# Kernel tuning notes

Hardware: AMD Instinct MI355X
Metric: run time of the kernel (lower is better)

Reference implementation:

```python
import jax, jax.numpy as jnp
import numpy as np

HQ, HKV, HD = 16, 4, 64  # q heads, kv heads, head dim
ROPE_BASE = 10000.0


def _rope_tables(n, dim):
    inv_freq = 1.0 / (ROPE_BASE ** (jnp.arange(0, dim, 2, dtype=jnp.float32) / dim))
    t = jnp.arange(n, dtype=jnp.float32)
    freqs = jnp.outer(t, inv_freq)           # [N, dim/2]
    emb = jnp.concatenate([freqs, freqs], -1)  # [N, dim]
    return jnp.cos(emb), jnp.sin(emb)


def _rotate_half(x):
    h = x.shape[-1] // 2
    return jnp.concatenate([-x[..., h:], x[..., :h]], axis=-1)


def _apply_rope(x, cos, sin):
    # x: [B, N, H, D]; cos/sin: [N, D]
    c = cos[None, :, None, :]
    s = sin[None, :, None, :]
    return x * c + _rotate_half(x) * s


def setup_inputs() -> dict:
    key = jax.random.key(0)
    ks = jax.random.split(key, 5)
    B, N, D = 2, 4096, 1024
    kvD = HKV * HD
    sc = 0.02
    return {
        "x": jax.random.normal(ks[0], (B, N, D), jnp.float32),
        "Wq": jax.random.normal(ks[1], (D, D), jnp.float32) * sc,
        "Wk": jax.random.normal(ks[2], (D, kvD), jnp.float32) * sc,
        "Wv": jax.random.normal(ks[3], (D, kvD), jnp.float32) * sc,
        "Wo": jax.random.normal(ks[4], (D, D), jnp.float32) * sc,
    }


def reference(x, Wq, Wk, Wv, Wo):
    B, N, D = x.shape
    G = HQ // HKV
    Q = (x @ Wq).reshape(B, N, HQ, HD)
    K = (x @ Wk).reshape(B, N, HKV, HD)
    V = (x @ Wv).reshape(B, N, HKV, HD)

    cos, sin = _rope_tables(N, HD)
    Q = _apply_rope(Q, cos, sin)
    K = _apply_rope(K, cos, sin)

    # GQA: expand KV heads to match Q heads (repeat_interleave over head dim)
    K = jnp.repeat(K, G, axis=2)  # [B, N, HQ, HD]
    V = jnp.repeat(V, G, axis=2)

    Q = Q.transpose(0, 2, 1, 3)  # [B, HQ, N, HD]
    K = K.transpose(0, 2, 1, 3)
    V = V.transpose(0, 2, 1, 3)

    scores = jnp.einsum('bhqd,bhkd->bhqk', Q, K) / jnp.sqrt(jnp.float32(HD))
    attn = jax.nn.softmax(scores, axis=-1)
    out = jnp.einsum('bhqk,bhkd->bhqd', attn, V)  # [B, HQ, N, HD]
    out = out.transpose(0, 2, 1, 3).reshape(B, N, D)
    return out @ Wo
```

## Files before the change

### kernel.cpp

```cpp
#include <hip/hip_runtime.h>

#define HQn   16
#define HKVn  4
#define HDn   64
#define SEQN  4096
#define NB    2
#define DM    1024
#define KVD   256
#define NPACK 1536

#define QSCALE 0.18033688011112042f

typedef __attribute__((ext_vector_type(8))) short short8;
typedef __attribute__((ext_vector_type(4))) float f32x4;

#define MFMA16 __builtin_amdgcn_mfma_f32_16x16x32_bf16
#define EXP2F(x) __builtin_amdgcn_exp2f(x)

static __device__ __forceinline__ unsigned short f2bf(float f){
  union { float f; unsigned int u; } c; c.f = f;
  unsigned int r = c.u + 0x7fffu + ((c.u >> 16) & 1u);
  return (unsigned short)(r >> 16);
}

#if __has_builtin(__builtin_amdgcn_cvt_pk_bf16_f32)
typedef __attribute__((ext_vector_type(2))) __bf16 bf16x2v;
static __device__ __forceinline__ unsigned int pk_bf2(float a, float b){
  union { bf16x2v v; unsigned int u; } c;
  c.v = __builtin_amdgcn_cvt_pk_bf16_f32(a, b);
  return c.u;
}
#else
static __device__ __forceinline__ unsigned int pk_bf2(float a, float b){
  union { float f; unsigned int u; } ca, cb; ca.f = a; cb.f = b;
  return ((ca.u + 0x8000u) >> 16) | ((cb.u + 0x8000u) & 0xFFFF0000u);
}
#endif

static __device__ __forceinline__ void gl2lds16(const void* g, void* l){
  __builtin_amdgcn_global_load_lds(
      (const __attribute__((address_space(1))) void*)g,
      (__attribute__((address_space(3))) void*)l, 16, 0, 0);
}

__global__ void rope_tables_k(float* __restrict__ ct, float* __restrict__ st){
  int t = blockIdx.x, d = threadIdx.x;
  int i = d & 31;
  float inv = 1.0f / powf(10000.0f, (float)i * (1.0f/32.0f));
  float ang = (float)t * inv;
  ct[t*HDn + d] = cosf(ang);
  st[t*HDn + d] = sinf(ang);
}

__global__ __launch_bounds__(256) void castx_k(const float* __restrict__ x,
                                               unsigned short* __restrict__ xb){
  size_t i = ((size_t)blockIdx.x * 256 + threadIdx.x) * 8;
  float4 a = *(const float4*)(x + i);
  float4 b = *(const float4*)(x + i + 4);
  short8 o;
  o[0]=f2bf(a.x); o[1]=f2bf(a.y); o[2]=f2bf(a.z); o[3]=f2bf(a.w);
  o[4]=f2bf(b.x); o[5]=f2bf(b.y); o[6]=f2bf(b.z); o[7]=f2bf(b.w);
  *(short8*)(xb + i) = o;
}

__global__ __launch_bounds__(256) void castw_k(
    const float* __restrict__ Wq, const float* __restrict__ Wk,
    const float* __restrict__ Wv, const float* __restrict__ Wo,
    unsigned short* __restrict__ Wqkv_t, unsigned short* __restrict__ Wot)
{
  const int z = blockIdx.z;
  const float* W; unsigned short* D; int srcN, nOff;
  if      (z == 0) { W = Wq; D = Wqkv_t; srcN = DM;  nOff = 0;    }
  else if (z == 1) { W = Wo; D = Wot;    srcN = DM;  nOff = 0;    }
  else if (z == 2) { W = Wk; D = Wqkv_t; srcN = KVD; nOff = 1024; }
  else             { W = Wv; D = Wqkv_t; srcN = KVD; nOff = 1280; }
  const int n0 = blockIdx.y * 64;
  if (n0 >= srcN) return;
  const int k0 = blockIdx.x * 64;
  const int tid = threadIdx.x;

  __shared__ float tile[64][65];
  const int lr = tid >> 4, lc = (tid & 15) * 4;
  #pragma unroll
  for (int p = 0; p < 4; p++) {
    float4 v = *(const float4*)&W[(size_t)(k0 + lr + p*16) * srcN + n0 + lc];
    tile[lr + p*16][lc+0] = v.x; tile[lr + p*16][lc+1] = v.y;
    tile[lr + p*16][lc+2] = v.z; tile[lr + p*16][lc+3] = v.w;
  }
  __syncthreads();

  const int nn = tid >> 2, kc = (tid & 3) * 16;
  unsigned short* dp = D + (size_t)(nOff + n0 + nn) * DM + k0 + kc;
  #pragma unroll
  for (int q = 0; q < 4; q++) {
    ushort4 o;
    o.x = f2bf(tile[kc + q*4 + 0][nn]);
    o.y = f2bf(tile[kc + q*4 + 1][nn]);
    o.z = f2bf(tile[kc + q*4 + 2][nn]);
    o.w = f2bf(tile[kc + q*4 + 3][nn]);
    *(ushort4*)(dp + q*4) = o;
  }
}

__global__ __launch_bounds__(256) void qkv2_k(
    const unsigned short* __restrict__ A, const unsigned short* __restrict__ Bt,
    const float* __restrict__ ct, const float* __restrict__ st,
    unsigned short* __restrict__ Qo, unsigned short* __restrict__ Ko,
    unsigned short* __restrict__ Vo)
{
  __shared__ __align__(16) short As[128][32];
  __shared__ __align__(16) short Bs[128][32];

  const int m0 = blockIdx.x * 128, n0 = blockIdx.y * 128;
  const int tid = threadIdx.x, lane = tid & 63, w = tid >> 6;
  const int wm = w >> 1, wn = w & 1;
  const int ln = lane & 15, quad = lane >> 4;

  f32x4 acc[4][4];
  #pragma unroll
  for (int i = 0; i < 4; i++)
    #pragma unroll
    for (int j = 0; j < 4; j++) acc[i][j] = (f32x4){0.f,0.f,0.f,0.f};

  const int r0 = tid >> 2, c8 = (tid & 3) * 8;
  const int r1 = r0 + 64;

  for (int k0 = 0; k0 < DM; k0 += 32) {
    gl2lds16(A  + (size_t)(m0 + r0)*DM + k0 + c8, &As[r0][c8]);
    gl2lds16(A  + (size_t)(m0 + r1)*DM + k0 + c8, &As[r1][c8]);
    gl2lds16(Bt + (size_t)(n0 + r0)*DM + k0 + c8, &Bs[r0][c8]);
    gl2lds16(Bt + (size_t)(n0 + r1)*DM + k0 + c8, &Bs[r1][c8]);
    __syncthreads();

    short8 af[4], bf[4];
    #pragma unroll
    for (int mb = 0; mb < 4; mb++) af[mb] = *(const short8*)&As[wm*64 + mb*16 + ln][quad*8];
    #pragma unroll
    for (int nb = 0; nb < 4; nb++) bf[nb] = *(const short8*)&Bs[wn*64 + nb*16 + ln][quad*8];
    #pragma unroll
    for (int mb = 0; mb < 4; mb++)
      #pragma unroll
      for (int nb = 0; nb < 4; nb++)
        acc[mb][nb] = MFMA16(af[mb], bf[nb], acc[mb][nb], 0, 0, 0);
    __syncthreads();
  }

  const int nc = n0 + wn*64;
  int kind, head;
  if (nc < 1024)      { kind = 0; head = nc >> 6;          }
  else if (nc < 1280) { kind = 1; head = (nc - 1024) >> 6; }
  else                { kind = 2; head = (nc - 1280) >> 6; }

  if (kind == 2) {
    #pragma unroll
    for (int mb = 0; mb < 4; mb++) {
      const int m = m0 + wm*64 + mb*16 + quad*4;
      const int t = m & (SEQN-1), b = m >> 12;
      #pragma unroll
      for (int nb = 0; nb < 4; nb++) {
        int d = nb*16 + ln;
        ushort4 pk;
        pk.x = f2bf(acc[mb][nb][0]); pk.y = f2bf(acc[mb][nb][1]);
        pk.z = f2bf(acc[mb][nb][2]); pk.w = f2bf(acc[mb][nb][3]);
        *(ushort4*)&Vo[(((size_t)(b*HKVn + head))*HDn + d)*SEQN + t] = pk;
      }
    }
  } else {
    #pragma unroll
    for (int mb = 0; mb < 4; mb++) {
      #pragma unroll
      for (int nb = 0; nb < 4; nb++) {
        #pragma unroll
        for (int r = 0; r < 4; r++) {
          int m = m0 + wm*64 + mb*16 + quad*4 + r;
          int t = m & (SEQN-1), b = m >> 12;
          int d = nb*16 + ln;
          float v = acc[mb][nb][r];
          float partner = (nb < 2) ? -acc[mb][nb+2][r] : acc[mb][nb-2][r];
          float cv = ct[t*HDn + d], sv = st[t*HDn + d];
          float o = v*cv + partner*sv;
          if (kind == 0) Qo[(((size_t)(b*HQn  + head))*SEQN + t)*HDn + d] = f2bf(o * QSCALE);
          else           Ko[(((size_t)(b*HKVn + head))*SEQN + t)*HDn + d] = f2bf(o);
        }
      }
    }
  }
}

__global__ __launch_bounds__(256, 4) void attn_k(
    const unsigned short* __restrict__ Q, const unsigned short* __restrict__ K,
    const unsigned short* __restrict__ Vt, unsigned short* __restrict__ AO)
{
  __shared__ __align__(16) short kb[2][64][64];
  __shared__ __align__(16) short vb[2][64][64];

  const int id  = blockIdx.x;
  const int bhv = id & 7;
  const int b   = bhv >> 2, hv = bhv & 3;
  const int rem = id >> 3;
  const int qt  = rem & 31;
  const int h   = hv*4 + (rem >> 5);
  const int q0  = qt * 128;

  const int tid = threadIdx.x, lane = tid & 63, w = tid >> 6;
  const int ln = lane & 15, quad = lane >> 4;

  const unsigned short* Qp = Q + (((size_t)(b*HQn + h))*SEQN + q0 + w*32) * HDn;
  const unsigned short* Kp = K + ((size_t)(b*HKVn + hv))*SEQN * HDn;
  const unsigned short* Vp = Vt + ((size_t)(b*HKVn + hv))*HDn * SEQN;

  short8 qf[2][2];
  qf[0][0] = *(const short8*)(Qp + ln*HDn + quad*8);
  qf[0][1] = *(const short8*)(Qp + ln*HDn + 32 + quad*8);
  qf[1][0] = *(const short8*)(Qp + (16+ln)*HDn + quad*8);
  qf[1][1] = *(const short8*)(Qp + (16+ln)*HDn + 32 + quad*8);

  short8 ones;
  #pragma unroll
  for (int j = 0; j < 8; j++) ones[j] = (short)0x3F80;

  f32x4 o[2][4], lacc[2];
  #pragma unroll
  for (int g = 0; g < 2; g++) {
    #pragma unroll
    for (int i = 0; i < 4; i++) o[g][i] = (f32x4){0.f,0.f,0.f,0.f};
    lacc[g] = (f32x4){0.f,0.f,0.f,0.f};
  }

  const int w2   = w & 1;
  const int lrow = lane >> 3;
  const int slin = lane & 7;
  const int sK   = slin ^ lrow;

  int kkey[4]; size_t vrow[4];
  #pragma unroll
  for (int i = 0; i < 4; i++) {
    kkey[i] = 32*w2 + 16*(i & 1) + 8*(lrow >> 2) + 4*(i >> 1) + (lrow & 3);
    vrow[i] = (size_t)(w2*32 + i*8 + lrow) * SEQN;
  }

  #define STAGE(cn, kts)                                                     \
    do {                                                                     \
      if (w < 2) {                                                           \
        _Pragma("unroll")                                                    \
        for (int i = 0; i < 4; i++)                                          \
          gl2lds16(Kp + (size_t)((kts) + kkey[i])*HDn + sK*8,                \
                   &kb[cn][w2*32 + i*8][0]);                                 \
      } else {                                                               \
        _Pragma("unroll")                                                    \
        for (int i = 0; i < 4; i++)                                          \
          gl2lds16(Vp + vrow[i] + (kts) + sK*8,                              \
                   &vb[cn][w2*32 + i*8][0]);                                 \
      }                                                                      \
    } while (0)

  const int swz0 = (( quad      ^ (ln & 7)) * 8);
  const int swz1 = (((quad + 4) ^ (ln & 7)) * 8);

  STAGE(0, 0);
  __syncthreads();

  int c = 0;
  for (int kt = 0; kt < SEQN; kt += 64) {
    if (kt + 64 < SEQN) STAGE(c ^ 1, kt + 64);

    f32x4 s[2][4];
    __builtin_amdgcn_s_setprio(1);
    #pragma unroll
    for (int nb = 0; nb < 4; nb++) {
      short8 k0 = *(const short8*)&kb[c][nb*16 + ln][swz0];
      short8 k1 = *(const short8*)&kb[c][nb*16 + ln][swz1];
      f32x4 t0 = (f32x4){0.f,0.f,0.f,0.f};
      t0 = MFMA16(k0, qf[0][0], t0, 0, 0, 0);
      t0 = MFMA16(k1, qf[0][1], t0, 0, 0, 0);
      s[0][nb] = t0;
      f32x4 t1 = (f32x4){0.f,0.f,0.f,0.f};
      t1 = MFMA16(k0, qf[1][0], t1, 0, 0, 0);
      t1 = MFMA16(k1, qf[1][1], t1, 0, 0, 0);
      s[1][nb] = t1;
    }
    __builtin_amdgcn_s_setprio(0);

    short8 pf[2][2];
    #pragma unroll
    for (int g = 0; g < 2; g++) {
      #pragma unroll
      for (int k2 = 0; k2 < 2; k2++) {
        union { short8 s8; unsigned u[4]; } f;
        f.u[0] = pk_bf2(EXP2F(s[g][2*k2  ][0]), EXP2F(s[g][2*k2  ][1]));
        f.u[1] = pk_bf2(EXP2F(s[g][2*k2  ][2]), EXP2F(s[g][2*k2  ][3]));
        f.u[2] = pk_bf2(EXP2F(s[g][2*k2+1][0]), EXP2F(s[g][2*k2+1][1]));
        f.u[3] = pk_bf2(EXP2F(s[g][2*k2+1][2]), EXP2F(s[g][2*k2+1][3]));
        pf[g][k2] = f.s8;
      }
    }

    __builtin_amdgcn_s_setprio(1);
    #pragma unroll
    for (int db = 0; db < 4; db++) {
      short8 v0 = *(const short8*)&vb[c][db*16 + ln][swz0];
      short8 v1 = *(const short8*)&vb[c][db*16 + ln][swz1];
      o[0][db] = MFMA16(pf[0][0], v0, o[0][db], 0, 0, 0);
      o[0][db] = MFMA16(pf[0][1], v1, o[0][db], 0, 0, 0);
      o[1][db] = MFMA16(pf[1][0], v0, o[1][db], 0, 0, 0);
      o[1][db] = MFMA16(pf[1][1], v1, o[1][db], 0, 0, 0);
    }
    lacc[0] = MFMA16(pf[0][0], ones, lacc[0], 0, 0, 0);
    lacc[0] = MFMA16(pf[0][1], ones, lacc[0], 0, 0, 0);
    lacc[1] = MFMA16(pf[1][0], ones, lacc[1], 0, 0, 0);
    lacc[1] = MFMA16(pf[1][1], ones, lacc[1], 0, 0, 0);
    __builtin_amdgcn_s_setprio(0);

    __syncthreads();
    c ^= 1;
  }
  #undef STAGE

  #pragma unroll
  for (int g = 0; g < 2; g++) {
    float inv[4];
    #pragma unroll
    for (int r = 0; r < 4; r++) inv[r] = 1.0f / lacc[g][r];
    #pragma unroll
    for (int db = 0; db < 4; db++) {
      #pragma unroll
      for (int r = 0; r < 4; r++) {
        int gq = q0 + w*32 + g*16 + quad*4 + r;
        int d  = db*16 + ln;
        AO[(((size_t)(b*SEQN + gq))*HQn + h)*HDn + d] = f2bf(o[g][db][r] * inv[r]);
      }
    }
  }
}

__global__ __launch_bounds__(256) void oproj2_k(
    const unsigned short* __restrict__ A, const unsigned short* __restrict__ Bt,
    float* __restrict__ out)
{
  __shared__ __align__(16) short As[128][32];
  __shared__ __align__(16) short Bs[128][32];

  const int m0 = blockIdx.x * 128, n0 = blockIdx.y * 128;
  const int tid = threadIdx.x, lane = tid & 63, w = tid >> 6;
  const int wm = w >> 1, wn = w & 1;
  const int ln = lane & 15, quad = lane >> 4;

  f32x4 acc[4][4];
  #pragma unroll
  for (int i = 0; i < 4; i++)
    #pragma unroll
    for (int j = 0; j < 4; j++) acc[i][j] = (f32x4){0.f,0.f,0.f,0.f};

  const int r0 = tid >> 2, c8 = (tid & 3) * 8;
  const int r1 = r0 + 64;

  for (int k0 = 0; k0 < DM; k0 += 32) {
    gl2lds16(A  + (size_t)(m0 + r0)*DM + k0 + c8, &As[r0][c8]);
    gl2lds16(A  + (size_t)(m0 + r1)*DM + k0 + c8, &As[r1][c8]);
    gl2lds16(Bt + (size_t)(n0 + r0)*DM + k0 + c8, &Bs[r0][c8]);
    gl2lds16(Bt + (size_t)(n0 + r1)*DM + k0 + c8, &Bs[r1][c8]);
    __syncthreads();

    short8 af[4], bf[4];
    #pragma unroll
    for (int mb = 0; mb < 4; mb++) af[mb] = *(const short8*)&As[wm*64 + mb*16 + ln][quad*8];
    #pragma unroll
    for (int nb = 0; nb < 4; nb++) bf[nb] = *(const short8*)&Bs[wn*64 + nb*16 + ln][quad*8];
    #pragma unroll
    for (int mb = 0; mb < 4; mb++)
      #pragma unroll
      for (int nb = 0; nb < 4; nb++)
        acc[mb][nb] = MFMA16(af[mb], bf[nb], acc[mb][nb], 0, 0, 0);
    __syncthreads();
  }

  #pragma unroll
  for (int mb = 0; mb < 4; mb++) {
    #pragma unroll
    for (int nb = 0; nb < 4; nb++) {
      #pragma unroll
      for (int r = 0; r < 4; r++) {
        int m = m0 + wm*64 + mb*16 + quad*4 + r;
        int c = n0 + wn*64 + nb*16 + ln;
        out[(size_t)m*DM + c] = acc[mb][nb][r];
      }
    }
  }
}

extern "C" void kernel_launch(void* const* d_in, const int* in_sizes, int n_in,
                              void* d_out, int out_size, void* d_ws, size_t ws_size,
                              hipStream_t stream) {
  const float* x  = (const float*)d_in[0];
  const float* Wq = (const float*)d_in[1];
  const float* Wk = (const float*)d_in[2];
  const float* Wv = (const float*)d_in[3];
  const float* Wo = (const float*)d_in[4];
  float* out = (float*)d_out;

  char* ws = (char*)d_ws;
  float* cos_t = (float*)ws;
  float* sin_t = cos_t + SEQN*HDn;
  unsigned short* xb     = (unsigned short*)(sin_t + SEQN*HDn);
  unsigned short* AO     = xb;
  unsigned short* Wqkv_t = xb + (size_t)NB*SEQN*DM;
  unsigned short* Wot    = Wqkv_t + (size_t)NPACK*DM;
  unsigned short* Qb     = Wot + (size_t)DM*DM;
  unsigned short* Kb     = Qb + (size_t)NB*HQn *SEQN*HDn;
  unsigned short* Vb     = Kb + (size_t)NB*HKVn*SEQN*HDn;

  hipLaunchKernelGGL(rope_tables_k, dim3(SEQN), dim3(HDn), 0, stream, cos_t, sin_t);
  hipLaunchKernelGGL(castx_k, dim3((NB*SEQN*DM)/(256*8)), dim3(256), 0, stream, x, xb);
  hipLaunchKernelGGL(castw_k, dim3(16, 16, 4), dim3(256), 0, stream,
                     Wq, Wk, Wv, Wo, Wqkv_t, Wot);
  hipLaunchKernelGGL(qkv2_k, dim3(64, 12), dim3(256), 0, stream,
                     xb, Wqkv_t, cos_t, sin_t, Qb, Kb, Vb);
  hipLaunchKernelGGL(attn_k, dim3(1024), dim3(256), 0, stream,
                     Qb, Kb, Vb, AO);
  hipLaunchKernelGGL(oproj2_k, dim3(64, 8), dim3(256), 0, stream,
                     AO, Wot, out);
}
```

Baseline: 314.9 us.

## Software-pipeline PV matmul one tile behind QK with triple-buffered V

```diff
diff --git a/kernel.cpp b/kernel.cpp
--- a/kernel.cpp
+++ b/kernel.cpp
@@ -192,7 +192,7 @@
     const unsigned short* __restrict__ Vt, unsigned short* __restrict__ AO)
 {
   __shared__ __align__(16) short kb[2][64][64];
-  __shared__ __align__(16) short vb[2][64][64];
+  __shared__ __align__(16) short vb[3][64][64];
 
   const int id  = blockIdx.x;
   const int bhv = id & 7;
@@ -239,37 +239,56 @@
     vrow[i] = (size_t)(w2*32 + i*8 + lrow) * SEQN;
   }
 
-  #define STAGE(cn, kts)                                                     \
+  #define STAGE(kcn, vcn, kts)                                               \
     do {                                                                     \
       if (w < 2) {                                                           \
         _Pragma("unroll")                                                    \
         for (int i = 0; i < 4; i++)                                          \
           gl2lds16(Kp + (size_t)((kts) + kkey[i])*HDn + sK*8,                \
-                   &kb[cn][w2*32 + i*8][0]);                                 \
+                   &kb[kcn][w2*32 + i*8][0]);                                \
       } else {                                                               \
         _Pragma("unroll")                                                    \
         for (int i = 0; i < 4; i++)                                          \
           gl2lds16(Vp + vrow[i] + (kts) + sK*8,                              \
-                   &vb[cn][w2*32 + i*8][0]);                                 \
+                   &vb[vcn][w2*32 + i*8][0]);                                \
       }                                                                      \
     } while (0)
 
+  #define PVSTEP(slot)                                                       \
+    do {                                                                     \
+      _Pragma("unroll")                                                      \
+      for (int db = 0; db < 4; db++) {                                       \
+        short8 v0 = *(const short8*)&vb[slot][db*16 + ln][swz0];             \
+        short8 v1 = *(const short8*)&vb[slot][db*16 + ln][swz1];             \
+        o[0][db] = MFMA16(pf[0][0], v0, o[0][db], 0, 0, 0);                  \
+        o[0][db] = MFMA16(pf[0][1], v1, o[0][db], 0, 0, 0);                  \
+        o[1][db] = MFMA16(pf[1][0], v0, o[1][db], 0, 0, 0);                  \
+        o[1][db] = MFMA16(pf[1][1], v1, o[1][db], 0, 0, 0);                  \
+      }                                                                      \
+      lacc[0] = MFMA16(pf[0][0], ones, lacc[0], 0, 0, 0);                    \
+      lacc[0] = MFMA16(pf[0][1], ones, lacc[0], 0, 0, 0);                    \
+      lacc[1] = MFMA16(pf[1][0], ones, lacc[1], 0, 0, 0);                    \
+      lacc[1] = MFMA16(pf[1][1], ones, lacc[1], 0, 0, 0);                    \
+    } while (0)
+
   const int swz0 = (( quad      ^ (ln & 7)) * 8);
   const int swz1 = (((quad + 4) ^ (ln & 7)) * 8);
 
-  STAGE(0, 0);
+  STAGE(0, 0, 0);
   __syncthreads();
 
-  int c = 0;
+  short8 pf[2][2];
+  int kc = 0, vprev = 2, vcur = 0, vnext = 1;
+
   for (int kt = 0; kt < SEQN; kt += 64) {
-    if (kt + 64 < SEQN) STAGE(c ^ 1, kt + 64);
-
+    if (kt + 64 < SEQN) STAGE(kc ^ 1, vnext, kt + 64);
+
+    __builtin_amdgcn_s_setprio(1);
     f32x4 s[2][4];
-    __builtin_amdgcn_s_setprio(1);
     #pragma unroll
     for (int nb = 0; nb < 4; nb++) {
-      short8 k0 = *(const short8*)&kb[c][nb*16 + ln][swz0];
-      short8 k1 = *(const short8*)&kb[c][nb*16 + ln][swz1];
+      short8 k0 = *(const short8*)&kb[kc][nb*16 + ln][swz0];
+      short8 k1 = *(const short8*)&kb[kc][nb*16 + ln][swz1];
       f32x4 t0 = (f32x4){0.f,0.f,0.f,0.f};
       t0 = MFMA16(k0, qf[0][0], t0, 0, 0, 0);
       t0 = MFMA16(k1, qf[0][1], t0, 0, 0, 0);
@@ -279,9 +298,10 @@
       t1 = MFMA16(k1, qf[1][1], t1, 0, 0, 0);
       s[1][nb] = t1;
     }
+
+    if (kt) PVSTEP(vprev);
     __builtin_amdgcn_s_setprio(0);
 
-    short8 pf[2][2];
     #pragma unroll
     for (int g = 0; g < 2; g++) {
       #pragma unroll
@@ -295,25 +315,15 @@
       }
     }
 
-    __builtin_amdgcn_s_setprio(1);
-    #pragma unroll
-    for (int db = 0; db < 4; db++) {
-      short8 v0 = *(const short8*)&vb[c][db*16 + ln][swz0];
-      short8 v1 = *(const short8*)&vb[c][db*16 + ln][swz1];
-      o[0][db] = MFMA16(pf[0][0], v0, o[0][db], 0, 0, 0);
-      o[0][db] = MFMA16(pf[0][1], v1, o[0][db], 0, 0, 0);
-      o[1][db] = MFMA16(pf[1][0], v0, o[1][db], 0, 0, 0);
-      o[1][db] = MFMA16(pf[1][1], v1, o[1][db], 0, 0, 0);
-    }
-    lacc[0] = MFMA16(pf[0][0], ones, lacc[0], 0, 0, 0);
-    lacc[0] = MFMA16(pf[0][1], ones, lacc[0], 0, 0, 0);
-    lacc[1] = MFMA16(pf[1][0], ones, lacc[1], 0, 0, 0);
-    lacc[1] = MFMA16(pf[1][1], ones, lacc[1], 0, 0, 0);
-    __builtin_amdgcn_s_setprio(0);
-
     __syncthreads();
-    c ^= 1;
-  }
+    kc ^= 1;
+    int tmp = vprev; vprev = vcur; vcur = vnext; vnext = tmp;
+  }
+
+  __builtin_amdgcn_s_setprio(1);
+  PVSTEP(vprev);
+  __builtin_amdgcn_s_setprio(0);
+  #undef PVSTEP
   #undef STAGE
 
   #pragma unroll
```

Result: slower. 339.6 us (+7.9%).
